# Optimization experiments

Hardware: AMD Instinct MI355X
Metric: run time of the kernel (lower is better)

## Reference

```python
import jax, jax.numpy as jnp
import numpy as np

D_SUMMARY = 128
N_LAYERS = 24
N_HEADS = 16
D_HEAD = 64
HIDDEN = 512
ACTIVE_MIN = 12
ROT = 16
THETA = 10000.0
B, P = 16, 128
L_ACT = N_LAYERS - ACTIVE_MIN
OUT_DIM = N_HEADS * 2 * D_HEAD


def setup_inputs() -> dict:
    key = jax.random.key(0)
    k1, k2, k3, k4, k5, k6 = jax.random.split(key, 6)
    summary_stack = jax.random.normal(k1, (B, P, D_SUMMARY), jnp.float32)
    positions = jnp.sort(jax.random.randint(k2, (P,), 0, 8192))
    s1 = 1.0 / np.sqrt(D_SUMMARY)
    s2 = 1.0 / np.sqrt(HIDDEN)
    W1 = jax.random.uniform(k3, (L_ACT, D_SUMMARY, HIDDEN), jnp.float32, -s1, s1)
    b1 = jax.random.uniform(k4, (L_ACT, HIDDEN), jnp.float32, -s1, s1)
    W2 = jax.random.uniform(k5, (L_ACT, HIDDEN, OUT_DIM), jnp.float32, -s2, s2)
    b2 = jax.random.uniform(k6, (L_ACT, OUT_DIM), jnp.float32, -s2, s2)
    return {"summary_stack": summary_stack, "positions": positions,
            "W1": W1, "b1": b1, "W2": W2, "b2": b2}


def reference(summary_stack, positions, W1, b1, W2, b2):
    # Batched 2-layer MLP across all active layers (grouped GEMM)
    h = jax.nn.relu(jnp.einsum('bps,lsh->lbph', summary_stack, W1) + b1[:, None, None, :])
    kv = jnp.einsum('lbph,lho->lbpo', h, W2) + b2[:, None, None, :]
    kv = kv.reshape(L_ACT, B, P, N_HEADS, 2, D_HEAD)
    k = jnp.transpose(kv[..., 0, :], (0, 1, 3, 2, 4))  # (L,B,H,P,D)
    v = jnp.transpose(kv[..., 1, :], (0, 1, 3, 2, 4))
    # RoPE on first ROT dims of K
    inv_freq = 1.0 / (THETA ** (jnp.arange(0, ROT, 2, dtype=jnp.float32) / ROT))
    freqs = positions.astype(jnp.float32)[:, None] * inv_freq[None, :]  # (P, ROT//2)
    emb = jnp.concatenate([freqs, freqs], axis=-1)  # (P, ROT)
    cos, sin = jnp.cos(emb), jnp.sin(emb)
    k_rot, k_pass = k[..., :ROT], k[..., ROT:]
    rot_half = jnp.concatenate([-k_rot[..., ROT // 2:], k_rot[..., :ROT // 2]], axis=-1)
    k_emb = k_rot * cos + rot_half * sin
    k = jnp.concatenate([k_emb, k_pass], axis=-1)
    # Inactive layers get zero K/V
    zeros = jnp.zeros((ACTIVE_MIN, B, N_HEADS, P, D_HEAD), k.dtype)
    k_all = jnp.concatenate([zeros, k], axis=0)
    v_all = jnp.concatenate([zeros, v], axis=0)
    return jnp.stack([k_all, v_all], axis=1)  # (n_layers, 2, B, H, P, D)
```

## Files before the change

kernel.cpp:

```cpp
#include <hip/hip_runtime.h>
#include <hip/hip_bf16.h>

#define L_ACT   12
#define BDIM    16
#define PDIM    128
#define DSUM    128
#define HID     512
#define ODIM    2048
#define NHEAD   16
#define DHEAD   64
#define MROWS   2048

typedef short short8 __attribute__((ext_vector_type(8)));
typedef float f32x4 __attribute__((ext_vector_type(4)));

__device__ __forceinline__ void gload_lds16(const __hip_bfloat16* g, __hip_bfloat16* l) {
  __builtin_amdgcn_global_load_lds(
      (const __attribute__((address_space(1))) unsigned int*)g,
      (__attribute__((address_space(3))) unsigned int*)l, 16, 0, 0);
}

__global__ __launch_bounds__(256) void prep_misc(
    const float* __restrict__ summary, const int* __restrict__ positions,
    __hip_bfloat16* __restrict__ A_bf, float* __restrict__ cs) {
  int i = blockIdx.x * 256 + threadIdx.x;
  A_bf[i] = __float2bfloat16(summary[i]);
  if (i < PDIM * 8) {
    int p = i >> 3, f = i & 7;
    double inv = pow(10000.0, -(double)f / 8.0);
    double ang = (double)positions[p] * inv;
    cs[i]        = (float)cos(ang);
    cs[1024 + i] = (float)sin(ang);
  }
}

__global__ __launch_bounds__(256) void transpose_bf16(
    const float* __restrict__ in, __hip_bfloat16* __restrict__ out, int J, int O) {
  __shared__ float t[32][33];
  int l = blockIdx.z;
  int o0 = blockIdx.x * 32, j0 = blockIdx.y * 32;
  int tx = threadIdx.x & 31, ty = threadIdx.x >> 5;
  const float* ip = in + (size_t)l * J * O;
#pragma unroll
  for (int r = 0; r < 32; r += 8)
    t[ty + r][tx] = ip[(size_t)(j0 + ty + r) * O + o0 + tx];
  __syncthreads();
  __hip_bfloat16* op = out + (size_t)l * J * O;
#pragma unroll
  for (int r = 0; r < 32; r += 8)
    op[(size_t)(o0 + ty + r) * J + j0 + tx] = __float2bfloat16(t[tx][ty + r]);
}

__global__ __launch_bounds__(256) void gemm1_128(
    const __hip_bfloat16* __restrict__ Aall,
    const __hip_bfloat16* __restrict__ Ball,
    const float* __restrict__ bias,
    __hip_bfloat16* __restrict__ Hall,
    f32x4* __restrict__ zeroBase) {
  const int KTOT = DSUM, NTOT = HID;
  __shared__ __hip_bfloat16 ldsA[128 * 64];
  __shared__ __hip_bfloat16 ldsB[128 * 64];
  const int l    = blockIdx.z;
  const int n0   = blockIdx.x * 128;
  const int m0   = blockIdx.y * 128;
  const int tid  = threadIdx.x;
  const int wid  = tid >> 6;
  const int lane = tid & 63;
  const int wr = wid >> 1, wc = wid & 1;
  const __hip_bfloat16* A  = Aall;
  const __hip_bfloat16* Bt = Ball + (size_t)l * NTOT * KTOT;

  f32x4 acc[4][4];
#pragma unroll
  for (int m = 0; m < 4; ++m)
#pragma unroll
    for (int n = 0; n < 4; ++n)
      acc[m][n] = {0.f, 0.f, 0.f, 0.f};

  const int srowi = lane >> 3;
  const int sblk  = (lane & 7) ^ srowi;

  for (int kt = 0; kt < KTOT / 64; ++kt) {
    __syncthreads();
#pragma unroll
    for (int s = 0; s < 4; ++s) {
      int seg = wid * 4 + s;
      int row = seg * 8 + srowi;
      gload_lds16(A  + (size_t)(m0 + row) * KTOT + kt * 64 + sblk * 8, ldsA + seg * 512);
      gload_lds16(Bt + (size_t)(n0 + row) * KTOT + kt * 64 + sblk * 8, ldsB + seg * 512);
    }
    __syncthreads();
#pragma unroll
    for (int kk = 0; kk < 2; ++kk) {
      short8 af[4], bfr[4];
#pragma unroll
      for (int m = 0; m < 4; ++m) {
        int row = wr * 64 + m * 16 + (lane & 15);
        int off = (kk * 64 + (lane >> 4) * 16) ^ ((row & 7) << 4);
        af[m] = *(const short8*)((const char*)ldsA + row * 128 + off);
      }
#pragma unroll
      for (int n = 0; n < 4; ++n) {
        int row = wc * 64 + n * 16 + (lane & 15);
        int off = (kk * 64 + (lane >> 4) * 16) ^ ((row & 7) << 4);
        bfr[n] = *(const short8*)((const char*)ldsB + row * 128 + off);
      }
#pragma unroll
      for (int m = 0; m < 4; ++m)
#pragma unroll
        for (int n = 0; n < 4; ++n)
          acc[m][n] = __builtin_amdgcn_mfma_f32_16x16x32_bf16(af[m], bfr[n], acc[m][n], 0, 0, 0);
    }
  }

  {
    const f32x4 z = {0.f, 0.f, 0.f, 0.f};
    int chunk = blockIdx.x + 4 * blockIdx.y + 64 * blockIdx.z;
    f32x4* zp = zeroBase + (size_t)chunk * 16384;
#pragma unroll
    for (int i = 0; i < 64; ++i)
      __builtin_nontemporal_store(z, zp + i * 256 + tid);
  }

  const int colBase = n0 + wc * 64 + (lane & 15);
  const int rowBase = m0 + wr * 64 + ((lane >> 4) << 2);
  __hip_bfloat16* H = Hall + (size_t)l * MROWS * HID;
#pragma unroll
  for (int n = 0; n < 4; ++n) {
    int col = colBase + n * 16;
    float bb = bias[l * NTOT + col];
#pragma unroll
    for (int m = 0; m < 4; ++m) {
      int row = rowBase + m * 16;
#pragma unroll
      for (int j = 0; j < 4; ++j) {
        float v = acc[m][n][j] + bb;
        v = v > 0.f ? v : 0.f;
        H[(size_t)(row + j) * HID + col] = __float2bfloat16(v);
      }
    }
  }
}

__global__ __launch_bounds__(512, 1) void gemm2_pipe(
    const __hip_bfloat16* __restrict__ Aall,
    const __hip_bfloat16* __restrict__ Ball,
    const float* __restrict__ bias,
    const float* __restrict__ cs,
    float* __restrict__ O) {
  __shared__ __hip_bfloat16 lds[4 * 16384];
  const int orig = blockIdx.x + 8 * blockIdx.y + 64 * blockIdx.z;
  const int nw   = (orig & 7) * 96 + (orig >> 3);
  const int bx   = nw & 7;
  const int by   = (nw >> 3) & 7;
  const int l    = nw >> 6;
  const int n0  = bx * 256;
  const int m0  = by * 256;
  const int tid = threadIdx.x;
  const int wid = tid >> 6, lane = tid & 63;
  const int wm  = wid >> 2, wn = wid & 3;
  const __hip_bfloat16* A  = Aall + (size_t)l * MROWS * HID;
  const __hip_bfloat16* Bt = Ball + (size_t)l * ODIM * HID;

  f32x4 acc[8][4];
#pragma unroll
  for (int m = 0; m < 8; ++m)
#pragma unroll
    for (int n = 0; n < 4; ++n)
      acc[m][n] = {0.f, 0.f, 0.f, 0.f};

  const int cidx0 = wid * 128 + lane;
  const int cidx1 = cidx0 + 64;
  const int r0 = cidx0 >> 2, c0 = (cidx0 & 3) ^ ((r0 >> 1) & 3);
  const int r1 = cidx1 >> 2, c1 = (cidx1 & 3) ^ ((r1 >> 1) & 3);

#define STAGE_A(slot, kt) do {                                                      \
    gload_lds16(A + (size_t)(m0 + r0) * HID + (kt) * 32 + c0 * 8,                   \
                lds + (slot) * 16384 + wid * 1024);                                 \
    gload_lds16(A + (size_t)(m0 + r1) * HID + (kt) * 32 + c1 * 8,                   \
                lds + (slot) * 16384 + wid * 1024 + 512);                           \
  } while (0)
#define STAGE_B(slot, kt) do {                                                      \
    gload_lds16(Bt + (size_t)(n0 + r0) * HID + (kt) * 32 + c0 * 8,                  \
                lds + (slot) * 16384 + 8192 + wid * 1024);                          \
    gload_lds16(Bt + (size_t)(n0 + r1) * HID + (kt) * 32 + c1 * 8,                  \
                lds + (slot) * 16384 + 8192 + wid * 1024 + 512);                    \
  } while (0)

  const int kq   = lane >> 4;
  const int rl15 = lane & 15;

#define LD_FRAG(dst, base, rr) do {                                                 \
    int r_ = (rr);                                                                  \
    int off_ = r_ * 64 + ((kq ^ ((r_ >> 1) & 3)) << 4);                             \
    dst = *(const short8*)((const char*)(base) + off_);                             \
  } while (0)

  STAGE_A(0, 0); STAGE_B(0, 0);
  STAGE_A(1, 1); STAGE_B(1, 1);
  STAGE_A(2, 2); STAGE_B(2, 2);
  asm volatile("s_waitcnt vmcnt(8)" ::: "memory");
  __builtin_amdgcn_s_barrier();

  const int NT = HID / 32;
  for (int t = 0; t < NT; ++t) {
    const __hip_bfloat16* sa = lds + (t & 3) * 16384;
    const __hip_bfloat16* sb = sa + 8192;
    short8 af[4], bfr[4];

#pragma unroll
    for (int n = 0; n < 4; ++n) LD_FRAG(bfr[n], sb, wn * 64 + n * 16 + rl15);
#pragma unroll
    for (int mi = 0; mi < 4; ++mi) LD_FRAG(af[mi], sa, wm * 128 + mi * 16 + rl15);
    if (t + 3 < NT) STAGE_A((t + 3) & 3, t + 3);
    __builtin_amdgcn_s_barrier();
    __builtin_amdgcn_s_setprio(1);
#pragma unroll
    for (int mi = 0; mi < 4; ++mi)
#pragma unroll
      for (int n = 0; n < 4; ++n)
        acc[mi][n] = __builtin_amdgcn_mfma_f32_16x16x32_bf16(af[mi], bfr[n], acc[mi][n], 0, 0, 0);
    __builtin_amdgcn_s_setprio(0);
    __builtin_amdgcn_s_barrier();

#pragma unroll
    for (int mi = 0; mi < 4; ++mi) LD_FRAG(af[mi], sa, wm * 128 + 64 + mi * 16 + rl15);
    if (t + 3 < NT) STAGE_B((t + 3) & 3, t + 3);
    __builtin_amdgcn_s_barrier();
    __builtin_amdgcn_s_setprio(1);
#pragma unroll
    for (int mi = 0; mi < 4; ++mi)
#pragma unroll
      for (int n = 0; n < 4; ++n)
        acc[4 + mi][n] = __builtin_amdgcn_mfma_f32_16x16x32_bf16(af[mi], bfr[n], acc[4 + mi][n], 0, 0, 0);
    __builtin_amdgcn_s_setprio(0);
    if (t < NT - 1) {
      if (t <= NT - 4)      asm volatile("s_waitcnt vmcnt(8)" ::: "memory");
      else if (t == NT - 3) asm volatile("s_waitcnt vmcnt(4)" ::: "memory");
      else                  asm volatile("s_waitcnt vmcnt(0)" ::: "memory");
    }
    __builtin_amdgcn_s_barrier();
  }
#undef STAGE_A
#undef STAGE_B
#undef LD_FRAG

  __syncthreads();
  const int head = bx * 2 + (wn >> 1);
  const int tkv  = wn & 1;
  const int bidx = by * 2 + wm;
  float* slab = O + ((((size_t)(l + L_ACT) * 2 + tkv) * BDIM + bidx) * NHEAD + head) * (PDIM * DHEAD);
  const bool ropeWave = (tkv == 0);

  float bb[4];
#pragma unroll
  for (int n = 0; n < 4; ++n) bb[n] = bias[l * ODIM + n0 + wn * 64 + n * 16 + rl15];

  float* Tw = (float*)lds + wid * 2080;

#pragma unroll
  for (int c = 0; c < 4; ++c) {
#pragma unroll
    for (int mh = 0; mh < 2; ++mh) {
      int mf = c * 2 + mh;
      int pl = mh * 16 + (lane >> 4) * 4;
#pragma unroll
      for (int n = 0; n < 4; ++n) {
#pragma unroll
        for (int j = 0; j < 4; ++j) {
          float v = acc[mf][n][j] + bb[n];
          if (ropeWave && n == 0) {
            float partner = __shfl_xor(v, 8);
            int p = c * 32 + pl + j;
            float cv = cs[p * 8 + (lane & 7)];
            float sv = cs[1024 + p * 8 + (lane & 7)];
            v = v * cv + (((lane & 15) < 8) ? -partner : partner) * sv;
          }
          Tw[(pl + j) * 65 + n * 16 + rl15] = v;
        }
      }
    }
#pragma unroll
    for (int it = 0; it < 8; ++it) {
      int pl = it * 4 + (lane >> 4);
      f32x4 vv = *(const f32x4*)(Tw + pl * 65 + rl15 * 4);
      __builtin_nontemporal_store(vv, (f32x4*)(slab + (size_t)(c * 32 + pl) * DHEAD + rl15 * 4));
    }
  }
}

extern "C" void kernel_launch(void* const* d_in, const int* in_sizes, int n_in,
                              void* d_out, int out_size, void* d_ws, size_t ws_size,
                              hipStream_t stream) {
  const float* summary   = (const float*)d_in[0];
  const int*   positions = (const int*)d_in[1];
  const float* W1 = (const float*)d_in[2];
  const float* b1 = (const float*)d_in[3];
  const float* W2 = (const float*)d_in[4];
  const float* b2 = (const float*)d_in[5];
  float* out = (float*)d_out;

  const size_t SCRATCH_BYTES = 52436992;
  char* sc = (ws_size >= SCRATCH_BYTES) ? (char*)d_ws : (char*)d_out;
  __hip_bfloat16* h_bf = (__hip_bfloat16*)sc;
  __hip_bfloat16* W2T  = (__hip_bfloat16*)(sc + 25165824);
  __hip_bfloat16* W1T  = (__hip_bfloat16*)(sc + 50331648);
  __hip_bfloat16* A_bf = (__hip_bfloat16*)(sc + 51904512);
  float*          cs   = (float*)(sc + 52428800);

  prep_misc<<<1024, 256, 0, stream>>>(summary, positions, A_bf, cs);
  transpose_bf16<<<dim3(512 / 32, 128 / 32, L_ACT), 256, 0, stream>>>(W1, W1T, 128, 512);
  transpose_bf16<<<dim3(2048 / 32, 512 / 32, L_ACT), 256, 0, stream>>>(W2, W2T, 512, 2048);

  gemm1_128<<<dim3(HID / 128, MROWS / 128, L_ACT), 256, 0, stream>>>(
      A_bf, W1T, b1, h_bf, (f32x4*)d_out);
  gemm2_pipe<<<dim3(ODIM / 256, MROWS / 256, L_ACT), 512, 0, stream>>>(h_bf, W2T, b2, cs, out);
}
```

Before: 141.0 us.

## Switch gemm2 to 32x32 MFMA, merge prep kernels, guard zero-fill for scratch fallback

Rewrites the main GEMM2 inner loop to use 32x32x16 bf16 MFMA tiles instead of 16x16x32, with matching LDS fragment loads and a reworked epilogue for the new accumulator layout, including RoPE. The three preprocessing launches (cast, cos/sin table, two weight transposes) are merged into one kernel to cut launch overhead. When the workspace is too small, the zero-fill of the inactive layers moves out of gemm1 into a separate kernel that runs after gemm2, so scratch placed in the output buffer is not clobbered early. Larger MFMA tiles aim for higher matrix-core throughput and fewer LDS reads per FLOP, at the cost of a more complex epilogue row mapping.

```diff
diff --git a/kernel.cpp b/kernel.cpp
--- a/kernel.cpp
+++ b/kernel.cpp
@@ -12,7 +12,8 @@
 #define MROWS   2048
 
 typedef short short8 __attribute__((ext_vector_type(8)));
-typedef float f32x4 __attribute__((ext_vector_type(4)));
+typedef float f32x4  __attribute__((ext_vector_type(4)));
+typedef float f32x16 __attribute__((ext_vector_type(16)));
 
 __device__ __forceinline__ void gload_lds16(const __hip_bfloat16* g, __hip_bfloat16* l) {
   __builtin_amdgcn_global_load_lds(
@@ -20,35 +21,54 @@
       (__attribute__((address_space(3))) unsigned int*)l, 16, 0, 0);
 }
 
-__global__ __launch_bounds__(256) void prep_misc(
-    const float* __restrict__ summary, const int* __restrict__ positions,
-    __hip_bfloat16* __restrict__ A_bf, float* __restrict__ cs) {
-  int i = blockIdx.x * 256 + threadIdx.x;
-  A_bf[i] = __float2bfloat16(summary[i]);
-  if (i < PDIM * 8) {
-    int p = i >> 3, f = i & 7;
-    double inv = pow(10000.0, -(double)f / 8.0);
-    double ang = (double)positions[p] * inv;
-    cs[i]        = (float)cos(ang);
-    cs[1024 + i] = (float)sin(ang);
-  }
-}
-
-__global__ __launch_bounds__(256) void transpose_bf16(
-    const float* __restrict__ in, __hip_bfloat16* __restrict__ out, int J, int O) {
+__global__ __launch_bounds__(256) void zerofill_kernel(f32x4* __restrict__ p, int n16) {
+  int stride = gridDim.x * 256;
+  for (int i = blockIdx.x * 256 + threadIdx.x; i < n16; i += stride)
+    p[i] = {0.f, 0.f, 0.f, 0.f};
+}
+
+__device__ __forceinline__ void transpose_tile(
+    const float* __restrict__ ip, __hip_bfloat16* __restrict__ op,
+    int J, int O, int o0, int j0, int tid) {
   __shared__ float t[32][33];
-  int l = blockIdx.z;
-  int o0 = blockIdx.x * 32, j0 = blockIdx.y * 32;
-  int tx = threadIdx.x & 31, ty = threadIdx.x >> 5;
-  const float* ip = in + (size_t)l * J * O;
+  int tx = tid & 31, ty = tid >> 5;
 #pragma unroll
   for (int r = 0; r < 32; r += 8)
     t[ty + r][tx] = ip[(size_t)(j0 + ty + r) * O + o0 + tx];
   __syncthreads();
-  __hip_bfloat16* op = out + (size_t)l * J * O;
 #pragma unroll
   for (int r = 0; r < 32; r += 8)
     op[(size_t)(o0 + ty + r) * J + j0 + tx] = __float2bfloat16(t[tx][ty + r]);
+}
+
+__global__ __launch_bounds__(256) void prep_all(
+    const float* __restrict__ summary, const int* __restrict__ positions,
+    const float* __restrict__ W1, const float* __restrict__ W2,
+    __hip_bfloat16* __restrict__ A_bf, float* __restrict__ cs,
+    __hip_bfloat16* __restrict__ W1T, __hip_bfloat16* __restrict__ W2T) {
+  const int bid = blockIdx.x;
+  const int tid = threadIdx.x;
+  if (bid < 1024) {
+    int i = bid * 256 + tid;
+    A_bf[i] = __float2bfloat16(summary[i]);
+    if (i < PDIM * 8) {
+      int p = i >> 3, f = i & 7;
+      double inv = pow(10000.0, -(double)f / 8.0);
+      double ang = (double)positions[p] * inv;
+      cs[i]        = (float)cos(ang);
+      cs[1024 + i] = (float)sin(ang);
+    }
+  } else if (bid < 1024 + 768) {
+    int idx = bid - 1024;
+    int bx = idx & 15, by = (idx >> 4) & 3, l = idx >> 6;
+    transpose_tile(W1 + (size_t)l * DSUM * HID, W1T + (size_t)l * DSUM * HID,
+                   DSUM, HID, bx * 32, by * 32, tid);
+  } else {
+    int idx = bid - 1792;
+    int bx = idx & 63, by = (idx >> 6) & 15, l = idx >> 10;
+    transpose_tile(W2 + (size_t)l * HID * ODIM, W2T + (size_t)l * HID * ODIM,
+                   HID, ODIM, bx * 32, by * 32, tid);
+  }
 }
 
 __global__ __launch_bounds__(256) void gemm1_128(
@@ -56,7 +76,7 @@
     const __hip_bfloat16* __restrict__ Ball,
     const float* __restrict__ bias,
     __hip_bfloat16* __restrict__ Hall,
-    f32x4* __restrict__ zeroBase) {
+    f32x4* __restrict__ zeroBase, int doZero) {
   const int KTOT = DSUM, NTOT = HID;
   __shared__ __hip_bfloat16 ldsA[128 * 64];
   __shared__ __hip_bfloat16 ldsB[128 * 64];
@@ -113,7 +133,7 @@
     }
   }
 
-  {
+  if (doZero) {
     const f32x4 z = {0.f, 0.f, 0.f, 0.f};
     int chunk = blockIdx.x + 4 * blockIdx.y + 64 * blockIdx.z;
     f32x4* zp = zeroBase + (size_t)chunk * 16384;
@@ -159,15 +179,17 @@
   const int tid = threadIdx.x;
   const int wid = tid >> 6, lane = tid & 63;
   const int wm  = wid >> 2, wn = wid & 3;
+  const int hi  = lane >> 5;
+  const int l31 = lane & 31;
   const __hip_bfloat16* A  = Aall + (size_t)l * MROWS * HID;
   const __hip_bfloat16* Bt = Ball + (size_t)l * ODIM * HID;
 
-  f32x4 acc[8][4];
-#pragma unroll
-  for (int m = 0; m < 8; ++m)
-#pragma unroll
-    for (int n = 0; n < 4; ++n)
-      acc[m][n] = {0.f, 0.f, 0.f, 0.f};
+  f32x16 acc[4][2];
+#pragma unroll
+  for (int m = 0; m < 4; ++m)
+#pragma unroll
+    for (int n = 0; n < 2; ++n)
+      acc[m][n] = (f32x16)(0.f);
 
   const int cidx0 = wid * 128 + lane;
   const int cidx1 = cidx0 + 64;
@@ -187,13 +209,10 @@
                 lds + (slot) * 16384 + 8192 + wid * 1024 + 512);                    \
   } while (0)
 
-  const int kq   = lane >> 4;
-  const int rl15 = lane & 15;
-
-#define LD_FRAG(dst, base, rr) do {                                                 \
-    int r_ = (rr);                                                                  \
-    int off_ = r_ * 64 + ((kq ^ ((r_ >> 1) & 3)) << 4);                             \
-    dst = *(const short8*)((const char*)(base) + off_);                             \
+#define LD32(dst, base, rowbase, kh) do {                                           \
+    int r_ = (rowbase) + l31;                                                       \
+    int c_ = (((kh) << 1) | hi) ^ ((r_ >> 1) & 3);                                  \
+    dst = *(const short8*)((const char*)(base) + r_ * 64 + (c_ << 4));              \
   } while (0)
 
   STAGE_A(0, 0); STAGE_B(0, 0);
@@ -206,33 +225,46 @@
   for (int t = 0; t < NT; ++t) {
     const __hip_bfloat16* sa = lds + (t & 3) * 16384;
     const __hip_bfloat16* sb = sa + 8192;
-    short8 af[4], bfr[4];
-
-#pragma unroll
-    for (int n = 0; n < 4; ++n) LD_FRAG(bfr[n], sb, wn * 64 + n * 16 + rl15);
-#pragma unroll
-    for (int mi = 0; mi < 4; ++mi) LD_FRAG(af[mi], sa, wm * 128 + mi * 16 + rl15);
+    short8 bfr[2][2], af[2][2];
+
+#pragma unroll
+    for (int ns = 0; ns < 2; ++ns)
+#pragma unroll
+      for (int kh = 0; kh < 2; ++kh)
+        LD32(bfr[ns][kh], sb, wn * 64 + ns * 32, kh);
+#pragma unroll
+    for (int ms = 0; ms < 2; ++ms)
+#pragma unroll
+      for (int kh = 0; kh < 2; ++kh)
+        LD32(af[ms][kh], sa, wm * 128 + ms * 32, kh);
     if (t + 3 < NT) STAGE_A((t + 3) & 3, t + 3);
     __builtin_amdgcn_s_barrier();
     __builtin_amdgcn_s_setprio(1);
 #pragma unroll
-    for (int mi = 0; mi < 4; ++mi)
-#pragma unroll
-      for (int n = 0; n < 4; ++n)
-        acc[mi][n] = __builtin_amdgcn_mfma_f32_16x16x32_bf16(af[mi], bfr[n], acc[mi][n], 0, 0, 0);
+    for (int ms = 0; ms < 2; ++ms)
+#pragma unroll
+      for (int ns = 0; ns < 2; ++ns) {
+        acc[ms][ns] = __builtin_amdgcn_mfma_f32_32x32x16_bf16(af[ms][0], bfr[ns][0], acc[ms][ns], 0, 0, 0);
+        acc[ms][ns] = __builtin_amdgcn_mfma_f32_32x32x16_bf16(af[ms][1], bfr[ns][1], acc[ms][ns], 0, 0, 0);
+      }
     __builtin_amdgcn_s_setprio(0);
     __builtin_amdgcn_s_barrier();
 
 #pragma unroll
-    for (int mi = 0; mi < 4; ++mi) LD_FRAG(af[mi], sa, wm * 128 + 64 + mi * 16 + rl15);
+    for (int ms = 0; ms < 2; ++ms)
+#pragma unroll
+      for (int kh = 0; kh < 2; ++kh)
+        LD32(af[ms][kh], sa, wm * 128 + 64 + ms * 32, kh);
     if (t + 3 < NT) STAGE_B((t + 3) & 3, t + 3);
     __builtin_amdgcn_s_barrier();
     __builtin_amdgcn_s_setprio(1);
 #pragma unroll
-    for (int mi = 0; mi < 4; ++mi)
-#pragma unroll
-      for (int n = 0; n < 4; ++n)
-        acc[4 + mi][n] = __builtin_amdgcn_mfma_f32_16x16x32_bf16(af[mi], bfr[n], acc[4 + mi][n], 0, 0, 0);
+    for (int ms = 0; ms < 2; ++ms)
+#pragma unroll
+      for (int ns = 0; ns < 2; ++ns) {
+        acc[2 + ms][ns] = __builtin_amdgcn_mfma_f32_32x32x16_bf16(af[ms][0], bfr[ns][0], acc[2 + ms][ns], 0, 0, 0);
+        acc[2 + ms][ns] = __builtin_amdgcn_mfma_f32_32x32x16_bf16(af[ms][1], bfr[ns][1], acc[2 + ms][ns], 0, 0, 0);
+      }
     __builtin_amdgcn_s_setprio(0);
     if (t < NT - 1) {
       if (t <= NT - 4)      asm volatile("s_waitcnt vmcnt(8)" ::: "memory");
@@ -243,7 +275,7 @@
   }
 #undef STAGE_A
 #undef STAGE_B
-#undef LD_FRAG
+#undef LD32
 
   __syncthreads();
   const int head = bx * 2 + (wn >> 1);
@@ -252,39 +284,37 @@
   float* slab = O + ((((size_t)(l + L_ACT) * 2 + tkv) * BDIM + bidx) * NHEAD + head) * (PDIM * DHEAD);
   const bool ropeWave = (tkv == 0);
 
-  float bb[4];
-#pragma unroll
-  for (int n = 0; n < 4; ++n) bb[n] = bias[l * ODIM + n0 + wn * 64 + n * 16 + rl15];
+  float bb[2];
+#pragma unroll
+  for (int ns = 0; ns < 2; ++ns) bb[ns] = bias[l * ODIM + n0 + wn * 64 + ns * 32 + l31];
 
   float* Tw = (float*)lds + wid * 2080;
-
-#pragma unroll
-  for (int c = 0; c < 4; ++c) {
-#pragma unroll
-    for (int mh = 0; mh < 2; ++mh) {
-      int mf = c * 2 + mh;
-      int pl = mh * 16 + (lane >> 4) * 4;
-#pragma unroll
-      for (int n = 0; n < 4; ++n) {
-#pragma unroll
-        for (int j = 0; j < 4; ++j) {
-          float v = acc[mf][n][j] + bb[n];
-          if (ropeWave && n == 0) {
-            float partner = __shfl_xor(v, 8);
-            int p = c * 32 + pl + j;
-            float cv = cs[p * 8 + (lane & 7)];
-            float sv = cs[1024 + p * 8 + (lane & 7)];
-            v = v * cv + (((lane & 15) < 8) ? -partner : partner) * sv;
-          }
-          Tw[(pl + j) * 65 + n * 16 + rl15] = v;
+  const int rl15 = lane & 15;
+
+#pragma unroll
+  for (int ms = 0; ms < 4; ++ms) {
+#pragma unroll
+    for (int ns = 0; ns < 2; ++ns) {
+#pragma unroll
+      for (int rg = 0; rg < 16; ++rg) {
+        int rowLocal = (rg & 3) + 8 * (rg >> 2) + 4 * hi;
+        float v = acc[ms][ns][rg] + bb[ns];
+        if (ropeWave && ns == 0) {
+          float partner = __shfl_xor(v, 8);
+          int p = ms * 32 + rowLocal;
+          float cv = cs[p * 8 + (lane & 7)];
+          float sv = cs[1024 + p * 8 + (lane & 7)];
+          float vr = v * cv + (((lane & 15) < 8) ? -partner : partner) * sv;
+          v = (l31 < 16) ? vr : v;
         }
+        Tw[rowLocal * 65 + ns * 32 + l31] = v;
       }
     }
 #pragma unroll
     for (int it = 0; it < 8; ++it) {
       int pl = it * 4 + (lane >> 4);
       f32x4 vv = *(const f32x4*)(Tw + pl * 65 + rl15 * 4);
-      __builtin_nontemporal_store(vv, (f32x4*)(slab + (size_t)(c * 32 + pl) * DHEAD + rl15 * 4));
+      __builtin_nontemporal_store(vv, (f32x4*)(slab + (size_t)(ms * 32 + pl) * DHEAD + rl15 * 4));
     }
   }
 }
@@ -301,18 +331,20 @@
   float* out = (float*)d_out;
 
   const size_t SCRATCH_BYTES = 52436992;
-  char* sc = (ws_size >= SCRATCH_BYTES) ? (char*)d_ws : (char*)d_out;
+  const bool useWs = (ws_size >= SCRATCH_BYTES);
+  char* sc = useWs ? (char*)d_ws : (char*)d_out;
   __hip_bfloat16* h_bf = (__hip_bfloat16*)sc;
   __hip_bfloat16* W2T  = (__hip_bfloat16*)(sc + 25165824);
   __hip_bfloat16* W1T  = (__hip_bfloat16*)(sc + 50331648);
   __hip_bfloat16* A_bf = (__hip_bfloat16*)(sc + 51904512);
   float*          cs   = (float*)(sc + 52428800);
 
-  prep_misc<<<1024, 256, 0, stream>>>(summary, positions, A_bf, cs);
-  transpose_bf16<<<dim3(512 / 32, 128 / 32, L_ACT), 256, 0, stream>>>(W1, W1T, 128, 512);
-  transpose_bf16<<<dim3(2048 / 32, 512 / 32, L_ACT), 256, 0, stream>>>(W2, W2T, 512, 2048);
+  prep_all<<<14080, 256, 0, stream>>>(summary, positions, W1, W2, A_bf, cs, W1T, W2T);
 
   gemm1_128<<<dim3(HID / 128, MROWS / 128, L_ACT), 256, 0, stream>>>(
-      A_bf, W1T, b1, h_bf, (f32x4*)d_out);
+      A_bf, W1T, b1, h_bf, (f32x4*)d_out, useWs ? 1 : 0);
   gemm2_pipe<<<dim3(ODIM / 256, MROWS / 256, L_ACT), 512, 0, stream>>>(h_bf, W2T, b2, cs, out);
-}
+
+  if (!useWs)
+    zerofill_kernel<<<2048, 256, 0, stream>>>((f32x4*)d_out, 12582912);
+}
```

New measurement: 150.8 us. 6.9% more time.

## Fuse W1 transpose into prep kernel and W2 transpose into gemm1 tail

Applied to the files above, without the earlier changes.

Merges the summary conversion, RoPE table and W1 transpose into one launch, and moves the W2 fp32-to-bf16 transpose into the tail of the gemm1 blocks. This cuts two kernel launches and lets the W2 transpose run alongside the first GEMM's work. Zeroing of the inactive output layers becomes conditional on workspace availability, with a separate zero-fill pass after gemm2 when scratch aliases the output. The risk is that gemm1 blocks get longer and serialized, since each one now also transposes 16 tiles of W2.

```diff
diff --git a/kernel.cpp b/kernel.cpp
--- a/kernel.cpp
+++ b/kernel.cpp
@@ -12,7 +12,7 @@
 #define MROWS   2048
 
 typedef short short8 __attribute__((ext_vector_type(8)));
-typedef float f32x4 __attribute__((ext_vector_type(4)));
+typedef float f32x4  __attribute__((ext_vector_type(4)));
 
 __device__ __forceinline__ void gload_lds16(const __hip_bfloat16* g, __hip_bfloat16* l) {
   __builtin_amdgcn_global_load_lds(
@@ -20,35 +20,45 @@
       (__attribute__((address_space(3))) unsigned int*)l, 16, 0, 0);
 }
 
-__global__ __launch_bounds__(256) void prep_misc(
+__global__ __launch_bounds__(256) void zerofill_kernel(f32x4* __restrict__ p, int n16) {
+  int stride = gridDim.x * 256;
+  for (int i = blockIdx.x * 256 + threadIdx.x; i < n16; i += stride)
+    p[i] = {0.f, 0.f, 0.f, 0.f};
+}
+
+__global__ __launch_bounds__(256) void prep_small(
     const float* __restrict__ summary, const int* __restrict__ positions,
-    __hip_bfloat16* __restrict__ A_bf, float* __restrict__ cs) {
-  int i = blockIdx.x * 256 + threadIdx.x;
-  A_bf[i] = __float2bfloat16(summary[i]);
-  if (i < PDIM * 8) {
-    int p = i >> 3, f = i & 7;
-    double inv = pow(10000.0, -(double)f / 8.0);
-    double ang = (double)positions[p] * inv;
-    cs[i]        = (float)cos(ang);
-    cs[1024 + i] = (float)sin(ang);
-  }
-}
-
-__global__ __launch_bounds__(256) void transpose_bf16(
-    const float* __restrict__ in, __hip_bfloat16* __restrict__ out, int J, int O) {
-  __shared__ float t[32][33];
-  int l = blockIdx.z;
-  int o0 = blockIdx.x * 32, j0 = blockIdx.y * 32;
-  int tx = threadIdx.x & 31, ty = threadIdx.x >> 5;
-  const float* ip = in + (size_t)l * J * O;
-#pragma unroll
-  for (int r = 0; r < 32; r += 8)
-    t[ty + r][tx] = ip[(size_t)(j0 + ty + r) * O + o0 + tx];
-  __syncthreads();
-  __hip_bfloat16* op = out + (size_t)l * J * O;
-#pragma unroll
-  for (int r = 0; r < 32; r += 8)
-    op[(size_t)(o0 + ty + r) * J + j0 + tx] = __float2bfloat16(t[tx][ty + r]);
+    const float* __restrict__ W1,
+    __hip_bfloat16* __restrict__ A_bf, float* __restrict__ cs,
+    __hip_bfloat16* __restrict__ W1T) {
+  const int bid = blockIdx.x;
+  const int tid = threadIdx.x;
+  if (bid < 1024) {
+    int i = bid * 256 + tid;
+    A_bf[i] = __float2bfloat16(summary[i]);
+    if (i < PDIM * 8) {
+      int p = i >> 3, f = i & 7;
+      double inv = pow(10000.0, -(double)f / 8.0);
+      double ang = (double)positions[p] * inv;
+      cs[i]        = (float)cos(ang);
+      cs[1024 + i] = (float)sin(ang);
+    }
+  } else {
+    __shared__ float t[32][33];
+    int idx = bid - 1024;
+    int bx = idx & 15, by = (idx >> 4) & 3, l = idx >> 6;
+    int o0 = bx * 32, j0 = by * 32;
+    int tx = tid & 31, ty = tid >> 5;
+    const float* ip = W1 + (size_t)l * DSUM * HID;
+#pragma unroll
+    for (int r = 0; r < 32; r += 8)
+      t[ty + r][tx] = ip[(size_t)(j0 + ty + r) * HID + o0 + tx];
+    __syncthreads();
+    __hip_bfloat16* op = W1T + (size_t)l * DSUM * HID;
+#pragma unroll
+    for (int r = 0; r < 32; r += 8)
+      op[(size_t)(o0 + ty + r) * DSUM + j0 + tx] = __float2bfloat16(t[tx][ty + r]);
+  }
 }
 
 __global__ __launch_bounds__(256) void gemm1_128(
@@ -56,7 +66,9 @@
     const __hip_bfloat16* __restrict__ Ball,
     const float* __restrict__ bias,
     __hip_bfloat16* __restrict__ Hall,
-    f32x4* __restrict__ zeroBase) {
+    const float* __restrict__ W2,
+    __hip_bfloat16* __restrict__ W2T,
+    f32x4* __restrict__ zeroBase, int doZero) {
   const int KTOT = DSUM, NTOT = HID;
   __shared__ __hip_bfloat16 ldsA[128 * 64];
   __shared__ __hip_bfloat16 ldsB[128 * 64];
@@ -113,10 +125,11 @@
     }
   }
 
-  {
+  const int bid = blockIdx.x + 4 * blockIdx.y + 64 * blockIdx.z;
+
+  if (doZero) {
     const f32x4 z = {0.f, 0.f, 0.f, 0.f};
-    int chunk = blockIdx.x + 4 * blockIdx.y + 64 * blockIdx.z;
-    f32x4* zp = zeroBase + (size_t)chunk * 16384;
+    f32x4* zp = zeroBase + (size_t)bid * 16384;
 #pragma unroll
     for (int i = 0; i < 64; ++i)
       __builtin_nontemporal_store(z, zp + i * 256 + tid);
@@ -138,6 +151,29 @@
         v = v > 0.f ? v : 0.f;
         H[(size_t)(row + j) * HID + col] = __float2bfloat16(v);
       }
+    }
+  }
+
+  {
+    float* tb = (float*)ldsA;
+    const int tx = tid & 31, ty = tid >> 5;
+    const int tbase = bid * 16;
+#pragma unroll 1
+    for (int tt = 0; tt < 16; ++tt) {
+      int t = tbase + tt;
+      int lz = t >> 10, rem = t & 1023;
+      int jt = rem >> 6, ot = rem & 63;
+      int j0 = jt * 32, o0 = ot * 32;
+      const float* ip = W2 + (size_t)lz * HID * ODIM;
+      __hip_bfloat16* op = W2T + (size_t)lz * HID * ODIM;
+      __syncthreads();
+#pragma unroll
+      for (int r = 0; r < 32; r += 8)
+        tb[(ty + r) * 33 + tx] = ip[(size_t)(j0 + ty + r) * ODIM + o0 + tx];
+      __syncthreads();
+#pragma unroll
+      for (int r = 0; r < 32; r += 8)
+        op[(size_t)(o0 + ty + r) * HID + j0 + tx] = __float2bfloat16(tb[tx * 33 + ty + r]);
     }
   }
 }
@@ -301,18 +337,20 @@
   float* out = (float*)d_out;
 
   const size_t SCRATCH_BYTES = 52436992;
-  char* sc = (ws_size >= SCRATCH_BYTES) ? (char*)d_ws : (char*)d_out;
+  const bool useWs = (ws_size >= SCRATCH_BYTES);
+  char* sc = useWs ? (char*)d_ws : (char*)d_out;
   __hip_bfloat16* h_bf = (__hip_bfloat16*)sc;
   __hip_bfloat16* W2T  = (__hip_bfloat16*)(sc + 25165824);
   __hip_bfloat16* W1T  = (__hip_bfloat16*)(sc + 50331648);
   __hip_bfloat16* A_bf = (__hip_bfloat16*)(sc + 51904512);
   float*          cs   = (float*)(sc + 52428800);
 
-  prep_misc<<<1024, 256, 0, stream>>>(summary, positions, A_bf, cs);
-  transpose_bf16<<<dim3(512 / 32, 128 / 32, L_ACT), 256, 0, stream>>>(W1, W1T, 128, 512);
-  transpose_bf16<<<dim3(2048 / 32, 512 / 32, L_ACT), 256, 0, stream>>>(W2, W2T, 512, 2048);
+  prep_small<<<1792, 256, 0, stream>>>(summary, positions, W1, A_bf, cs, W1T);
 
   gemm1_128<<<dim3(HID / 128, MROWS / 128, L_ACT), 256, 0, stream>>>(
-      A_bf, W1T, b1, h_bf, (f32x4*)d_out);
+      A_bf, W1T, b1, h_bf, W2, W2T, (f32x4*)d_out, useWs ? 1 : 0);
   gemm2_pipe<<<dim3(ODIM / 256, MROWS / 256, L_ACT), 512, 0, stream>>>(h_bf, W2T, b2, cs, out);
-}
+
+  if (!useWs)
+    zerofill_kernel<<<2048, 256, 0, stream>>>((f32x4*)d_out, 12582912);
+}
```

After: 136.7 us. -3.1%, faster.
